# Performance work log

Hardware: AMD Instinct MI355X
Metric: run time of the kernel (lower is better)

Reference implementation:

```python
import jax, jax.numpy as jnp
import numpy as np
import math

WINDOW = 11
CHANNEL = 3
PAD = WINDOW // 2
C1 = 0.01 ** 2
C2 = 0.03 ** 2


def gaussian_kernel(size, sigma):
    tmp = np.arange(size).astype(np.float32) - size // 2
    k1 = 1 / (sigma * math.sqrt(2 * math.pi)) * np.exp(-0.5 * (tmp / sigma) ** 2)
    k2 = np.outer(k1, k1)
    return (k2 / k2.sum()).astype(np.float32)


def setup_inputs() -> dict:
    key = jax.random.key(0)
    k1, k2 = jax.random.split(key)
    img1 = jax.random.uniform(k1, (16, CHANNEL, 512, 512), dtype=jnp.float32)
    img2 = jax.random.uniform(k2, (16, CHANNEL, 512, 512), dtype=jnp.float32)
    kern2d = gaussian_kernel(WINDOW, 1.5)  # [11,11]
    kernel = jnp.asarray(np.broadcast_to(kern2d[None, None], (CHANNEL, 1, WINDOW, WINDOW)).copy())
    return {"img1": img1, "img2": img2, "kernel": kernel}


def _blur(x, kernel):
    # depthwise conv2d, SAME padding via explicit pad=5 on each side
    return jax.lax.conv_general_dilated(
        x, kernel,
        window_strides=(1, 1),
        padding=((PAD, PAD), (PAD, PAD)),
        dimension_numbers=("NCHW", "OIHW", "NCHW"),
        feature_group_count=CHANNEL,
    )


def reference(img1, img2, kernel):
    mu1 = _blur(img1, kernel)
    mu2 = _blur(img2, kernel)
    mu1_sq = mu1 * mu1
    mu2_sq = mu2 * mu2
    mu1_mu2 = mu1 * mu2
    sigma1_sq = _blur(img1 * img1, kernel) - mu1_sq
    sigma2_sq = _blur(img2 * img2, kernel) - mu2_sq
    sigma12 = _blur(img1 * img2, kernel) - mu1_mu2
    ssim_map = (2 * mu1_mu2 + C1) * (2 * sigma12 + C2) / (
        (mu1_sq + mu2_sq + C1) * (sigma1_sq + sigma2_sq + C2))
    return ssim_map.mean()
```

## Files before the change

kernel.cpp:

```cpp
#include <hip/hip_runtime.h>


#define IMG_H 512
#define IMG_W 512
#define N_PLANES 48
#define KW 11
#define BLOCK 256
#define WAVE_COLS 64
#define STRIP_H 64
#define BLOCKS_X (IMG_W / (WAVE_COLS * 4))
#define BLOCKS_Y (IMG_H / STRIP_H)
#define NBLK (N_PLANES * BLOCKS_X * BLOCKS_Y)
#define PAIRF 320
#define C1_CONST 1.0e-4f
#define C2_CONST 9.0e-4f

typedef float v2f __attribute__((ext_vector_type(2)));
typedef float v4f __attribute__((ext_vector_type(4)));

typedef const __attribute__((address_space(1))) void GV;
typedef __attribute__((address_space(3))) void LV;

__device__ __forceinline__ void dma16(const float* g, float* l) {
  __builtin_amdgcn_global_load_lds((GV*)g, (LV*)l, 16, 0, 0);
}

__device__ __forceinline__ float bcastf(float x) {
  return __uint_as_float(__builtin_amdgcn_readfirstlane(__float_as_uint(x)));
}

#define VLO(V) __builtin_shufflevector(V, V, 0, 1)
#define VHI(V) __builtin_shufflevector(V, V, 2, 3)

#define PTAP(WJ, X1, X2) { \
    const v2f t1_ = (WJ) * (X1); const v2f t2_ = (WJ) * (X2); \
    M1 += t1_; M2 += t2_; \
    QS += t1_ * (X1); QS += t2_ * (X2); Q12 += t1_ * (X2); }

#define HPASS(ROW, SLOT, BP) { \
  if ((ROW) >= 0 && (ROW) < IMG_H) { \
    const float* s1_ = (BP); const float* s2_ = (BP) + 80; \
    v2f M1 = {0.f,0.f}, M2 = {0.f,0.f}, QS = {0.f,0.f}, Q12 = {0.f,0.f}; \
    { const v4f A0 = *(const v4f*)(s1_ + a); \
      const v4f B0 = *(const v4f*)(s2_ + a); \
      const v4f A1 = *(const v4f*)(s1_ + a + 4); \
      const v4f B1 = *(const v4f*)(s2_ + a + 4); \
      PTAP(Wp2[0], VLO(A0), VLO(B0)) PTAP(Wp2[1], VHI(A0), VHI(B0)) \
      PTAP(Wp2[2], VLO(A1), VLO(B1)) PTAP(Wp2[3], VHI(A1), VHI(B1)) } \
    { const v4f A2 = *(const v4f*)(s1_ + a + 8); \
      const v4f B2 = *(const v4f*)(s2_ + a + 8); \
      const v2f A3 = *(const v2f*)(s1_ + a + 12); \
      const v2f B3 = *(const v2f*)(s2_ + a + 12); \
      PTAP(Wp2[4], VLO(A2), VLO(B2)) PTAP(Wp2[5], VHI(A2), VHI(B2)) \
      PTAP(Wp2[6], A3, B3) } \
    Pm[(SLOT)] = (v2f){M1.x + M1.y, M2.x + M2.y}; \
    Pq[(SLOT)] = (v2f){QS.x + QS.y, Q12.x + Q12.y}; \
  } else { \
    Pm[(SLOT)] = (v2f){0.f, 0.f}; Pq[(SLOT)] = (v2f){0.f, 0.f}; } }

#define EMT(K, QQ) { const float w_ = wkr[(K)]; \
    vmP += w_ * Pm[(QQ)]; vqP += w_ * Pq[(QQ)]; }

#define EMITQ(OFF) { \
  v2f vmP = {0.f,0.f}, vqP = {0.f,0.f}; \
  EMT(0, ((OFF)+0)%12)  EMT(1, ((OFF)+1)%12)  EMT(2, ((OFF)+2)%12) \
  EMT(3, ((OFF)+3)%12)  EMT(4, ((OFF)+4)%12)  EMT(5, ((OFF)+5)%12) \
  EMT(6, ((OFF)+6)%12)  EMT(7, ((OFF)+7)%12)  EMT(8, ((OFF)+8)%12) \
  EMT(9, ((OFF)+9)%12)  EMT(10, ((OFF)+10)%12) \
  const float vm1_ = vmP.x, vm2_ = vmP.y, vqs_ = vqP.x, vq12_ = vqP.y; \
  const float mu11_ = vm1_ * vm1_; \
  const float mu22_ = vm2_ * vm2_; \
  const float mu12_ = vm1_ * vm2_; \
  const float musum_ = mu11_ + mu22_; \
  const float sigs_  = vqs_  - musum_; \
  const float sig12_ = vq12_ - mu12_; \
  const float num_ = (2.f * mu12_ + C1_CONST) * (2.f * sig12_ + C2_CONST); \
  const float den_ = (musum_ + C1_CONST) * (sigs_ + C2_CONST); \
  acc += num_ * __builtin_amdgcn_rcpf(den_); }

#define STEP2(P, EMIT) { \
  { const int na_ = gr+4 < 0 ? 0 : (gr+4 > IMG_H-1 ? IMG_H-1 : gr+4); \
    const int nb_ = gr+5 < 0 ? 0 : (gr+5 > IMG_H-1 ? IMG_H-1 : gr+5); \
    if (lane < 40) { \
      float* d_ = slw + (((P)+2)%3) * PAIRF; \
      dma16(srcbase + (size_t)na_ * IMG_W, d_); \
      dma16(srcbase + (size_t)nb_ * IMG_W, d_ + 160); } } \
  if (EMIT) { EMITQ((2*(P))%12) EMITQ((2*(P)+1)%12) } \
  asm volatile("s_waitcnt vmcnt(4)" ::: "memory"); \
  __builtin_amdgcn_sched_barrier(0); \
  { const float* bp_ = slw + ((P)%3) * PAIRF; \
    HPASS(gr,     (2*(P))%12,     bp_) \
    HPASS(gr + 1, (2*(P)+1)%12,   bp_ + 160) } \
  gr += 2; }

__global__ __launch_bounds__(BLOCK) void ssim_strip_kernel(
    const float* __restrict__ img1,
    const float* __restrict__ img2,
    const float* __restrict__ kern2d,
    float* __restrict__ partial)
{
  __shared__ __align__(16) float slice[4][3][PAIRF];
  __shared__ float wk_lds[KW];
  __shared__ float wave_sums[BLOCK / 64];

  const int tid  = threadIdx.x;
  const int wid  = tid >> 6;
  const int lane = tid & 63;

  if (tid < KW) {
    float s = 0.f;
    #pragma unroll
    for (int j = 0; j < KW; ++j) s += kern2d[tid * KW + j];
    wk_lds[tid] = s;
  }
  __syncthreads();

  float wkr[KW];
  #pragma unroll
  for (int k = 0; k < KW; ++k) wkr[k] = bcastf(wk_lds[k]);

  const int bid   = blockIdx.x;
  const int plane = bid / (BLOCKS_X * BLOCKS_Y);
  const int srem  = bid % (BLOCKS_X * BLOCKS_Y);
  const int y0    = (srem / BLOCKS_X) * STRIP_H;
  const int x0b   = (srem % BLOCKS_X) * (WAVE_COLS * 4);
  const float* __restrict__ p1 = img1 + (size_t)plane * IMG_H * IMG_W;
  const float* __restrict__ p2 = img2 + (size_t)plane * IMG_H * IMG_W;

  const int x0w   = x0b + wid * WAVE_COLS;
  const int gx    = x0w + lane;
  const int wbase = x0w - 8;

  const int a = (lane + 3) & ~3;
  const int r = (lane + 3) & 3;

  v2f Wp2[7];
  #pragma unroll
  for (int j = 0; j < 7; ++j) {
    float w0, w1;
    {
      const int e = 2 * j;
      const int k = e - r;
      const int col = wbase + a + e;
      w0 = (k >= 0 && k <= 10 && col >= 0 && col < IMG_W) ? wk_lds[k] : 0.f;
    }
    {
      const int e = 2 * j + 1;
      const int k = e - r;
      const int col = wbase + a + e;
      w1 = (k >= 0 && k <= 10 && col >= 0 && col < IMG_W) ? wk_lds[k] : 0.f;
    }
    Wp2[j] = (v2f){w0, w1};
  }

  const int li  = lane < 20 ? lane : lane - 20;
  const int c0r = wbase + 4 * li;
  const int c0  = c0r < 0 ? 0 : (c0r > IMG_W - 4 ? IMG_W - 4 : c0r);
  const float* srcbase = (lane < 20 ? p1 : p2) + c0;

  float* slw = &slice[wid][0][0];

  v2f Pm[12], Pq[12];
  float acc = 0.f;
  int gr = y0 - 5;

  {
    const int q0 = gr     < 0 ? 0 : gr;
    const int q1 = gr + 1 < 0 ? 0 : gr + 1;
    const int q2 = gr + 2 < 0 ? 0 : gr + 2;
    const int q3 = gr + 3 < 0 ? 0 : gr + 3;
    if (lane < 40) {
      dma16(srcbase + (size_t)q0 * IMG_W, slw);
      dma16(srcbase + (size_t)q1 * IMG_W, slw + 160);
      dma16(srcbase + (size_t)q2 * IMG_W, slw + PAIRF);
      dma16(srcbase + (size_t)q3 * IMG_W, slw + PAIRF + 160);
    }
  }

  STEP2(0, 0) STEP2(1, 0) STEP2(2, 0) STEP2(3, 0) STEP2(4, 0) STEP2(5, 0)
  #pragma unroll 1
  for (int it = 0; it < 5; ++it) {
    STEP2(0, 1) STEP2(1, 1) STEP2(2, 1) STEP2(3, 1) STEP2(4, 1) STEP2(5, 1)
  }
  STEP2(0, 1)
  { EMITQ(2) EMITQ(3) }

  #pragma unroll
  for (int off = 32; off > 0; off >>= 1)
    acc += __shfl_down(acc, off, 64);
  if ((tid & 63) == 0) wave_sums[tid >> 6] = acc;
  __syncthreads();
  if (tid == 0)
    partial[bid] = wave_sums[0] + wave_sums[1] + wave_sums[2] + wave_sums[3];
}

__global__ __launch_bounds__(256) void ssim_reduce_kernel(
    const float* __restrict__ partial, float* __restrict__ out)
{
  const int tid = threadIdx.x;
  double acc = 0.0;
  for (int i = tid; i < NBLK; i += 256) acc += (double)partial[i];
  #pragma unroll
  for (int off = 32; off > 0; off >>= 1)
    acc += __shfl_down(acc, off, 64);
  __shared__ double wsums[4];
  if ((tid & 63) == 0) wsums[tid >> 6] = acc;
  __syncthreads();
  if (tid == 0) {
    const double total = wsums[0] + wsums[1] + wsums[2] + wsums[3];
    const double inv_n = 1.0 / ((double)N_PLANES * IMG_H * IMG_W);
    out[0] = (float)(total * inv_n);
  }
}

extern "C" void kernel_launch(void* const* d_in, const int* in_sizes, int n_in,
                              void* d_out, int out_size, void* d_ws, size_t ws_size,
                              hipStream_t stream)
{
  const float* img1 = (const float*)d_in[0];
  const float* img2 = (const float*)d_in[1];
  const float* kern = (const float*)d_in[2];
  float* out = (float*)d_out;
  float* partial = (float*)d_ws;

  ssim_strip_kernel<<<NBLK, BLOCK, 0, stream>>>(img1, img2, kern, partial);
  ssim_reduce_kernel<<<1, 256, 0, stream>>>(partial, out);
}
```

Baseline: 56.84 us.

## Precompute squared-sum and product rows in LDS to cut horizontal-pass arithmetic

Adds a staging step in which each wave computes x1²+x2² and x1·x2 for the next raw row pair. It writes them into a new double-buffered LDS area, so the horizontal 11-tap pass becomes four FMAs per tap instead of two multiplies plus five accumulate ops. This is meant to cut VALU work in the inner filter. In exchange, the horizontal pass now reads twice as much LDS and needs extra LDS writes. The vmcnt wait drops from 4 to 2 so the row pair after the current one has landed before staging, which shortens the effective prefetch distance.

```diff
diff --git a/kernel.cpp b/kernel.cpp
--- a/kernel.cpp
+++ b/kernel.cpp
@@ -12,6 +12,7 @@
 #define BLOCKS_Y (IMG_H / STRIP_H)
 #define NBLK (N_PLANES * BLOCKS_X * BLOCKS_Y)
 #define PAIRF 320
+#define SPF   320
 #define C1_CONST 1.0e-4f
 #define C2_CONST 9.0e-4f
 
@@ -32,27 +33,49 @@
 #define VLO(V) __builtin_shufflevector(V, V, 0, 1)
 #define VHI(V) __builtin_shufflevector(V, V, 2, 3)
 
-#define PTAP(WJ, X1, X2) { \
-    const v2f t1_ = (WJ) * (X1); const v2f t2_ = (WJ) * (X2); \
-    M1 += t1_; M2 += t2_; \
-    QS += t1_ * (X1); QS += t2_ * (X2); Q12 += t1_ * (X2); }
-
-#define HPASS(ROW, SLOT, BP) { \
+#define PTAP4(WJ, X1, X2, SS, PP) { \
+    M1 += (WJ) * (X1); M2 += (WJ) * (X2); \
+    QS += (WJ) * (SS); Q12 += (WJ) * (PP); }
+
+#define SPSTAGE(RAWBP, SPBP) { \
+  if (lane < 40) { \
+    const float* rb_ = (RAWBP) + sprow; \
+    float*       sb_ = (SPBP) + sprow; \
+    const v4f X1_ = *(const v4f*)(rb_); \
+    const v4f X2_ = *(const v4f*)(rb_ + 80); \
+    const v4f S4_ = X1_ * X1_ + X2_ * X2_; \
+    const v4f P4_ = X1_ * X2_; \
+    *(v4f*)(sb_)      = S4_; \
+    *(v4f*)(sb_ + 80) = P4_; } }
+
+#define HPASS(ROW, SLOT, RB, SB) { \
   if ((ROW) >= 0 && (ROW) < IMG_H) { \
-    const float* s1_ = (BP); const float* s2_ = (BP) + 80; \
+    const float* s1_ = (RB); const float* s2_ = (RB) + 80; \
+    const float* ss_ = (SB); const float* pp_ = (SB) + 80; \
     v2f M1 = {0.f,0.f}, M2 = {0.f,0.f}, QS = {0.f,0.f}, Q12 = {0.f,0.f}; \
-    { const v4f A0 = *(const v4f*)(s1_ + a); \
-      const v4f B0 = *(const v4f*)(s2_ + a); \
-      const v4f A1 = *(const v4f*)(s1_ + a + 4); \
-      const v4f B1 = *(const v4f*)(s2_ + a + 4); \
-      PTAP(Wp2[0], VLO(A0), VLO(B0)) PTAP(Wp2[1], VHI(A0), VHI(B0)) \
-      PTAP(Wp2[2], VLO(A1), VLO(B1)) PTAP(Wp2[3], VHI(A1), VHI(B1)) } \
-    { const v4f A2 = *(const v4f*)(s1_ + a + 8); \
-      const v4f B2 = *(const v4f*)(s2_ + a + 8); \
-      const v2f A3 = *(const v2f*)(s1_ + a + 12); \
-      const v2f B3 = *(const v2f*)(s2_ + a + 12); \
-      PTAP(Wp2[4], VLO(A2), VLO(B2)) PTAP(Wp2[5], VHI(A2), VHI(B2)) \
-      PTAP(Wp2[6], A3, B3) } \
+    { const v4f X1 = *(const v4f*)(s1_ + a); \
+      const v4f X2 = *(const v4f*)(s2_ + a); \
+      const v4f SS = *(const v4f*)(ss_ + a); \
+      const v4f PP = *(const v4f*)(pp_ + a); \
+      PTAP4(Wp2[0], VLO(X1), VLO(X2), VLO(SS), VLO(PP)) \
+      PTAP4(Wp2[1], VHI(X1), VHI(X2), VHI(SS), VHI(PP)) } \
+    { const v4f X1 = *(const v4f*)(s1_ + a + 4); \
+      const v4f X2 = *(const v4f*)(s2_ + a + 4); \
+      const v4f SS = *(const v4f*)(ss_ + a + 4); \
+      const v4f PP = *(const v4f*)(pp_ + a + 4); \
+      PTAP4(Wp2[2], VLO(X1), VLO(X2), VLO(SS), VLO(PP)) \
+      PTAP4(Wp2[3], VHI(X1), VHI(X2), VHI(SS), VHI(PP)) } \
+    { const v4f X1 = *(const v4f*)(s1_ + a + 8); \
+      const v4f X2 = *(const v4f*)(s2_ + a + 8); \
+      const v4f SS = *(const v4f*)(ss_ + a + 8); \
+      const v4f PP = *(const v4f*)(pp_ + a + 8); \
+      PTAP4(Wp2[4], VLO(X1), VLO(X2), VLO(SS), VLO(PP)) \
+      PTAP4(Wp2[5], VHI(X1), VHI(X2), VHI(SS), VHI(PP)) } \
+    { const v2f X1 = *(const v2f*)(s1_ + a + 12); \
+      const v2f X2 = *(const v2f*)(s2_ + a + 12); \
+      const v2f SS = *(const v2f*)(ss_ + a + 12); \
+      const v2f PP = *(const v2f*)(pp_ + a + 12); \
+      PTAP4(Wp2[6], X1, X2, SS, PP) } \
     Pm[(SLOT)] = (v2f){M1.x + M1.y, M2.x + M2.y}; \
     Pq[(SLOT)] = (v2f){QS.x + QS.y, Q12.x + Q12.y}; \
   } else { \
@@ -82,15 +105,17 @@
   { const int na_ = gr+4 < 0 ? 0 : (gr+4 > IMG_H-1 ? IMG_H-1 : gr+4); \
     const int nb_ = gr+5 < 0 ? 0 : (gr+5 > IMG_H-1 ? IMG_H-1 : gr+5); \
     if (lane < 40) { \
-      float* d_ = slw + (((P)+2)%3) * PAIRF; \
+      float* d_ = raww + (((P)+2)%3) * PAIRF; \
       dma16(srcbase + (size_t)na_ * IMG_W, d_); \
       dma16(srcbase + (size_t)nb_ * IMG_W, d_ + 160); } } \
   if (EMIT) { EMITQ((2*(P))%12) EMITQ((2*(P)+1)%12) } \
-  asm volatile("s_waitcnt vmcnt(4)" ::: "memory"); \
+  asm volatile("s_waitcnt vmcnt(2)" ::: "memory"); \
   __builtin_amdgcn_sched_barrier(0); \
-  { const float* bp_ = slw + ((P)%3) * PAIRF; \
-    HPASS(gr,     (2*(P))%12,     bp_) \
-    HPASS(gr + 1, (2*(P)+1)%12,   bp_ + 160) } \
+  SPSTAGE(raww + (((P)+1)%3) * PAIRF, spw + (((P)+1)%2) * SPF) \
+  { const float* rb_ = raww + ((P)%3) * PAIRF; \
+    const float* sb_ = spw  + ((P)%2) * SPF; \
+    HPASS(gr,     (2*(P))%12,   rb_,       sb_) \
+    HPASS(gr + 1, (2*(P)+1)%12, rb_ + 160, sb_ + 160) } \
   gr += 2; }
 
 __global__ __launch_bounds__(BLOCK) void ssim_strip_kernel(
@@ -99,7 +124,8 @@
     const float* __restrict__ kern2d,
     float* __restrict__ partial)
 {
-  __shared__ __align__(16) float slice[4][3][PAIRF];
+  __shared__ __align__(16) float slice_raw[4][3][PAIRF];
+  __shared__ __align__(16) float slice_sp[4][2][SPF];
   __shared__ float wk_lds[KW];
   __shared__ float wave_sums[BLOCK / 64];
 
@@ -128,10 +154,9 @@
   const float* __restrict__ p2 = img2 + (size_t)plane * IMG_H * IMG_W;
 
   const int x0w   = x0b + wid * WAVE_COLS;
-  const int gx    = x0w + lane;
   const int wbase = x0w - 8;
 
-  const int a = (lane + 3) & ~3;
+  const int a = ((lane & 63) + 3) & ~3;
   const int r = (lane + 3) & 3;
 
   v2f Wp2[7];
@@ -158,7 +183,10 @@
   const int c0  = c0r < 0 ? 0 : (c0r > IMG_W - 4 ? IMG_W - 4 : c0r);
   const float* srcbase = (lane < 20 ? p1 : p2) + c0;
 
-  float* slw = &slice[wid][0][0];
+  const int sprow = (lane < 20 ? 0 : 160) + 4 * li;
+
+  float* raww = &slice_raw[wid][0][0];
+  float* spw  = &slice_sp[wid][0][0];
 
   v2f Pm[12], Pq[12];
   float acc = 0.f;
@@ -170,12 +198,15 @@
     const int q2 = gr + 2 < 0 ? 0 : gr + 2;
     const int q3 = gr + 3 < 0 ? 0 : gr + 3;
     if (lane < 40) {
-      dma16(srcbase + (size_t)q0 * IMG_W, slw);
-      dma16(srcbase + (size_t)q1 * IMG_W, slw + 160);
-      dma16(srcbase + (size_t)q2 * IMG_W, slw + PAIRF);
-      dma16(srcbase + (size_t)q3 * IMG_W, slw + PAIRF + 160);
+      dma16(srcbase + (size_t)q0 * IMG_W, raww);
+      dma16(srcbase + (size_t)q1 * IMG_W, raww + 160);
+      dma16(srcbase + (size_t)q2 * IMG_W, raww + PAIRF);
+      dma16(srcbase + (size_t)q3 * IMG_W, raww + PAIRF + 160);
     }
   }
+  asm volatile("s_waitcnt vmcnt(2)" ::: "memory");
+  __builtin_amdgcn_sched_barrier(0);
+  SPSTAGE(raww, spw)
 
   STEP2(0, 0) STEP2(1, 0) STEP2(2, 0) STEP2(3, 0) STEP2(4, 0) STEP2(5, 0)
   #pragma unroll 1
```

Result: slower. 83.82 us (+47.5%).
